# Performance work log

Hardware: AMD Instinct MI355X
Metric: run time of the kernel (lower is better)

The kernel has to match this reference:

```python
import jax, jax.numpy as jnp
import numpy as np

# Mamba2 defaults (mamba_ssm): d_state=128, d_conv=4, expand=2, headdim=64, ngroups=1
NB, D_MODEL, D_STATE, D_CONV, HEADDIM = 2, 512, 128, 4, 64
D_INNER = 2 * D_MODEL                      # expand * d_model
NHEADS = D_INNER // HEADDIM                # 16
CONV_DIM = D_INNER + 2 * D_STATE           # x, B, C go through depthwise conv
D_IN_PROJ = 2 * D_INNER + 2 * D_STATE + NHEADS  # z, xBC, dt
VOCAB, LABEL, B, L = 32000, 1000, 2, 512


def setup_inputs() -> dict:
    key = jax.random.key(0)
    ks = jax.random.split(key, 8)
    nrm = lambda k, shape, s: jax.random.normal(k, shape, dtype=jnp.float32) * s
    tokens = jax.random.randint(ks[0], (B, L), 0, VOCAB)
    embedding = nrm(ks[1], (VOCAB, D_MODEL), 0.02)
    in_proj_w = nrm(ks[2], (NB, D_IN_PROJ, D_MODEL), D_MODEL ** -0.5)
    conv_w = nrm(ks[3], (NB, CONV_DIM, D_CONV), D_CONV ** -0.5)
    conv_b = jnp.zeros((NB, CONV_DIM), jnp.float32)
    # dt_bias = inverse-softplus of dt ~ logUniform[1e-3, 0.1] (Mamba2 init)
    dt = jnp.exp(jax.random.uniform(ks[4], (NB, NHEADS), minval=float(np.log(1e-3)), maxval=float(np.log(0.1))))
    dt_bias = dt + jnp.log(-jnp.expm1(-dt))
    A_log = jnp.log(jax.random.uniform(ks[5], (NB, NHEADS), minval=1.0, maxval=16.0))
    D = jnp.ones((NB, NHEADS), jnp.float32)
    rms_w = jnp.ones((NB, D_INNER), jnp.float32)
    out_proj_w = nrm(ks[6], (NB, D_MODEL, D_INNER), D_INNER ** -0.5)
    ln_w = jnp.ones((NB, D_MODEL), jnp.float32)
    ln_b = jnp.zeros((NB, D_MODEL), jnp.float32)
    head_w = nrm(ks[7], (LABEL, D_MODEL), D_MODEL ** -0.5)
    head_b = jnp.zeros((LABEL,), jnp.float32)
    return dict(tokens=tokens, embedding=embedding, in_proj_w=in_proj_w, conv_w=conv_w,
                conv_b=conv_b, dt_bias=dt_bias, A_log=A_log, D=D, rms_w=rms_w,
                out_proj_w=out_proj_w, ln_w=ln_w, ln_b=ln_b, head_w=head_w, head_b=head_b)


def _mamba2(u, Wi, cw, cb, dtb, Alog, Dv, rw, Wo):
    b, l, _ = u.shape
    zxbcdt = u @ Wi.T                                  # (b,l,D_IN_PROJ)
    z = zxbcdt[..., :D_INNER]
    xBC = zxbcdt[..., D_INNER:D_INNER + CONV_DIM]
    dt = jax.nn.softplus(zxbcdt[..., D_INNER + CONV_DIM:] + dtb)   # (b,l,h)
    # causal depthwise conv1d, kernel size D_CONV
    xp = jnp.pad(xBC, ((0, 0), (D_CONV - 1, 0), (0, 0)))
    xBC = sum(xp[:, k:k + l, :] * cw[:, k] for k in range(D_CONV)) + cb
    xBC = jax.nn.silu(xBC)
    xh = xBC[..., :D_INNER].reshape(b, l, NHEADS, HEADDIM)
    Bm = xBC[..., D_INNER:D_INNER + D_STATE]           # (b,l,n), ngroups=1
    Cm = xBC[..., D_INNER + D_STATE:]                  # (b,l,n)
    A = -jnp.exp(Alog)                                 # (h,)
    dA = jnp.exp(dt * A)                               # (b,l,h)

    def step(h, inp):
        dA_t, dt_t, x_t, B_t, C_t = inp                # (b,h),(b,h),(b,h,p),(b,n),(b,n)
        h = h * dA_t[:, :, None, None] + (dt_t[:, :, None] * x_t)[..., None] * B_t[:, None, None, :]
        return h, jnp.einsum('bhpn,bn->bhp', h, C_t)

    h0 = jnp.zeros((b, NHEADS, HEADDIM, D_STATE), u.dtype)
    inp = (jnp.swapaxes(dA, 0, 1), jnp.swapaxes(dt, 0, 1), jnp.swapaxes(xh, 0, 1),
           jnp.swapaxes(Bm, 0, 1), jnp.swapaxes(Cm, 0, 1))
    _, ys = jax.lax.scan(step, h0, inp)
    y = jnp.swapaxes(ys, 0, 1) + Dv[:, None] * xh      # (b,l,h,p)
    # gated RMSNorm (norm_before_gate=False): normalize y*silu(z)
    y = y.reshape(b, l, D_INNER) * jax.nn.silu(z)
    y = y * jax.lax.rsqrt(jnp.mean(y * y, -1, keepdims=True) + 1e-5) * rw
    return y @ Wo.T


def _layernorm(x, w, bias):
    mu = jnp.mean(x, -1, keepdims=True)
    xc = x - mu
    var = jnp.mean(xc * xc, -1, keepdims=True)
    return xc * jax.lax.rsqrt(var + 1e-5) * w + bias


def reference(tokens, embedding, in_proj_w, conv_w, conv_b, dt_bias, A_log, D,
              rms_w, out_proj_w, ln_w, ln_b, head_w, head_b):
    x = embedding[tokens]                              # (b,l,d)
    for i in range(NB):
        y = _mamba2(x, in_proj_w[i], conv_w[i], conv_b[i], dt_bias[i],
                    A_log[i], D[i], rms_w[i], out_proj_w[i])
        x = _layernorm(y + x, ln_w[i], ln_b[i])        # residual + LN (dropout=identity)
    return x @ head_w.T + head_b                        # (b,l,label)
```

## Files before the change

kernel.cpp:

```cpp
#include <hip/hip_runtime.h>

#define L_SEQ 512
#define BATCH 2
#define NROWS (BATCH*L_SEQ)
#define DMODEL 512
#define DINNER 1024
#define DSTATE 128
#define NHEADSM 16
#define CONVD 1280
#define DINPROJ 2320
#define QCH 32
#define NCH 16
#define WI_PAD 2368
#define WH_PAD 1024

#define W_CONVW 0
#define W_CONVB 10240
#define W_DTB   12800
#define W_ALOG  12832
#define W_DD    12864
#define W_RMSW  12896
#define W_LNW   14944
#define W_LNB   15968
#define W_HEADB 16992
#define O_X     18048
#define O_ZX    (O_X  + NROWS*DMODEL)
#define O_XC    (O_ZX + NROWS*DINPROJ)
#define O_DT    (O_XC + NROWS*CONVD)
#define O_Y     (O_DT + NROWS*NHEADSM)
#define O_O     (O_Y  + NROWS*DINNER)
#define O_LA    (O_O  + NROWS*DMODEL)
#define O_S     (O_LA + 16384)
#define O_UB    (O_S  + 4194304)
#define U_WI   0
#define U_WO   2424832
#define U_WH   3473408
#define U_XBF  3997696
#define U_YBF  4521984

#define NSMALL 17992
#define NPREPW (2*WI_PAD + 2*DMODEL + WH_PAD)

typedef __attribute__((ext_vector_type(8))) short short8;
typedef __attribute__((ext_vector_type(4))) float floatx4;

__device__ __forceinline__ float b2f(unsigned short h){ return __uint_as_float(((unsigned)h)<<16); }
__device__ __forceinline__ unsigned short f2b(float x){
  unsigned u = __float_as_uint(x);
  return (unsigned short)((u + 0x7fffu + ((u>>16)&1u)) >> 16);
}
__device__ __forceinline__ float loadIn(const void* p, long i, int f){
  return f ? b2f(((const unsigned short*)p)[i]) : ((const float*)p)[i];
}

__global__ void k_detect(const unsigned* __restrict__ emb, int* __restrict__ flag){
  __shared__ int red[256];
  int t = threadIdx.x; int cnt = 0;
  for (int i = 0; i < 16; i++){
    unsigned w = emb[t*16 + i];
    unsigned e = (w >> 7) & 0xffu;
    cnt += (e >= 100 && e <= 126) ? 1 : 0;
  }
  red[t] = cnt; __syncthreads();
  if (t == 0){
    int s = 0;
    for (int i = 0; i < 256; i++) s += red[i];
    *flag = (s > 2048) ? 1 : 0;
  }
}

struct ConvArgs { const void* src[9]; int off[10]; };

__global__ void k_prep(ConvArgs a, const void* __restrict__ wi, const void* __restrict__ wo,
                       const void* __restrict__ wh, const int* __restrict__ tok,
                       const void* __restrict__ emb, const int* __restrict__ flag,
                       float* __restrict__ dstSmall,
                       unsigned short* __restrict__ WiB, unsigned short* __restrict__ WoB,
                       unsigned short* __restrict__ WhB,
                       float* __restrict__ x, unsigned short* __restrict__ xbf)
{
  int f = *flag;
  int blk = blockIdx.x;
  if (blk < 71){
    int i = blk*256 + threadIdx.x;
    if (i < a.off[9]){
      int s = 0;
      while (i >= a.off[s+1]) s++;
      dstSmall[i] = loadIn(a.src[s], i - a.off[s], f);
    }
    return;
  }
  blk -= 71;
  if (blk < NPREPW){
    int r = blk;
    const void* src = nullptr; unsigned short* dst; long sb = 0, db; int K; bool zero = false;
    if (r < 2*WI_PAD){
      int layer = r / WI_PAD, row = r % WI_PAD;
      K = DMODEL; dst = WiB; db = ((long)layer*WI_PAD + row)*DMODEL;
      if (row < DINPROJ){ src = wi; sb = ((long)layer*DINPROJ + row)*DMODEL; } else zero = true;
    } else if (r < 2*WI_PAD + 2*DMODEL){
      int rr = r - 2*WI_PAD;
      K = DINNER; dst = WoB; db = (long)rr*DINNER;
      src = wo; sb = db;
    } else {
      int row = r - 2*WI_PAD - 2*DMODEL;
      K = DMODEL; dst = WhB; db = (long)row*DMODEL;
      if (row < 1000){ src = wh; sb = db; } else zero = true;
    }
    for (int c = threadIdx.x; c < K; c += 256)
      dst[db + c] = zero ? (unsigned short)0
                         : (f ? ((const unsigned short*)src)[sb + c] : f2b(((const float*)src)[sb + c]));
    return;
  }
  int r = blk - NPREPW;
  long base = (long)tok[r] * DMODEL;
  for (int c = threadIdx.x; c < DMODEL; c += 256){
    float v = loadIn(emb, base + c, f);
    x[(long)r*DMODEL + c] = v;
    xbf[(long)r*DMODEL + c] = f ? ((const unsigned short*)emb)[base + c] : f2b(v);
  }
}

__global__ __launch_bounds__(256) void k_mfma_nt(
    const unsigned short* __restrict__ A, const unsigned short* __restrict__ B,
    void* __restrict__ C, int M, int N, int K,
    const float* __restrict__ bias, const int* __restrict__ flag, int outDual)
{
  __shared__ unsigned short As[4096];
  __shared__ unsigned short Bs[4096];
  int f = *flag;
  int t = threadIdx.x;
  int w = t >> 6, lane = t & 63;
  int quad = lane >> 4, l16 = lane & 15;
  int m0 = blockIdx.y << 6, n0 = blockIdx.x << 6;
  int wm = (w & 1) << 5, wn = (w >> 1) << 5;
  floatx4 acc[2][2];
  #pragma unroll
  for (int mi = 0; mi < 2; mi++)
    #pragma unroll
    for (int ni = 0; ni < 2; ni++) acc[mi][ni] = (floatx4){0.f,0.f,0.f,0.f};

  int idx0 = (w << 7) + lane;
  int r0s = idx0 >> 3, g0 = idx0 & 7;
  int idx1 = idx0 + 64;
  int r1s = idx1 >> 3, g1 = idx1 & 7;
  long aOff0 = (long)(m0 + r0s)*K + g0*8;
  long aOff1 = (long)(m0 + r1s)*K + g1*8;
  long bOff0 = (long)(n0 + r0s)*K + g0*8;
  long bOff1 = (long)(n0 + r1s)*K + g1*8;
  int w0 = r0s*64 + (g0 ^ (r0s & 7))*8;
  int w1 = r1s*64 + (g1 ^ (r1s & 7))*8;

  for (int k0 = 0; k0 < K; k0 += 64){
    short8 a0 = *(const short8*)&A[aOff0 + k0];
    short8 a1 = *(const short8*)&A[aOff1 + k0];
    short8 b0 = *(const short8*)&B[bOff0 + k0];
    short8 b1 = *(const short8*)&B[bOff1 + k0];
    __syncthreads();
    *(short8*)&As[w0] = a0; *(short8*)&As[w1] = a1;
    *(short8*)&Bs[w0] = b0; *(short8*)&Bs[w1] = b1;
    __syncthreads();
    #pragma unroll
    for (int ks = 0; ks < 2; ks++){
      short8 af[2], bfr[2];
      #pragma unroll
      for (int mi = 0; mi < 2; mi++){
        int r = wm + mi*16 + l16;
        int pos = ((ks << 2) + quad) ^ (r & 7);
        af[mi] = *(const short8*)&As[r*64 + pos*8];
      }
      #pragma unroll
      for (int ni = 0; ni < 2; ni++){
        int r = wn + ni*16 + l16;
        int pos = ((ks << 2) + quad) ^ (r & 7);
        bfr[ni] = *(const short8*)&Bs[r*64 + pos*8];
      }
      #pragma unroll
      for (int mi = 0; mi < 2; mi++)
        #pragma unroll
        for (int ni = 0; ni < 2; ni++)
          acc[mi][ni] = __builtin_amdgcn_mfma_f32_16x16x32_bf16(af[mi], bfr[ni], acc[mi][ni], 0, 0, 0);
    }
  }
  #pragma unroll
  for (int mi = 0; mi < 2; mi++)
    #pragma unroll
    for (int ni = 0; ni < 2; ni++){
      int col = n0 + wn + ni*16 + l16;
      if (col >= N) continue;
      float bv = bias ? bias[col] : 0.f;
      #pragma unroll
      for (int rr = 0; rr < 4; rr++){
        int row = m0 + wm + mi*16 + (quad << 2) + rr;
        float v = acc[mi][ni][rr] + bv;
        long idx = (long)row*N + col;
        if (outDual && f) ((unsigned short*)C)[idx] = f2b(v);
        else              ((float*)C)[idx] = v;
      }
    }
}

__global__ __launch_bounds__(256) void k_conv_dt(
    const float* __restrict__ zx, const float* __restrict__ cw, const float* __restrict__ cb,
    const float* __restrict__ dtb, float* __restrict__ xc, float* __restrict__ dt)
{
  int r = blockIdx.x; int b = r >> 9, l = r & 511;
  int t = threadIdx.x;
  for (int c = t; c < CONVD; c += 256){
    float s = cb[c];
    #pragma unroll
    for (int k = 0; k < 4; k++){
      int pos = l - 3 + k;
      if (pos >= 0)
        s = fmaf(zx[(long)(b*L_SEQ + pos)*DINPROJ + DINNER + c], cw[c*4 + k], s);
    }
    xc[(long)r*CONVD + c] = s / (1.f + __expf(-s));
  }
  if (t < NHEADSM){
    float v = zx[(long)r*DINPROJ + DINNER + CONVD + t] + dtb[t];
    dt[r*NHEADSM + t] = (v > 20.f) ? v : log1pf(__expf(v));
  }
}

__global__ __launch_bounds__(256) void k_chunk1(
    const float* __restrict__ xc, const float* __restrict__ dtbuf,
    const float* __restrict__ alog, const float* __restrict__ dvec,
    float* __restrict__ S, float* __restrict__ LAb, float* __restrict__ y)
{
  int c = blockIdx.x, h = blockIdx.y, b = blockIdx.z;
  int t = threadIdx.x, w = t >> 6, lane = t & 63;
  int quad = lane >> 4, l16 = lane & 15;
  int l0 = c*QCH;
  __shared__ unsigned short XT[64*40];
  __shared__ unsigned short BTc[128*40];
  __shared__ unsigned short Bb[32*136];
  __shared__ unsigned short Cb[32*136];
  __shared__ unsigned short Gb[32*40];
  __shared__ float dtl[32], lal[32], coef[32];
  float A  = -__expf(alog[h]);
  float Dv = dvec[h];

  float xv[8];
  #pragma unroll
  for (int k = 0; k < 8; k++){
    int idx = t + k*256; int j = idx >> 6, p = idx & 63;
    xv[k] = xc[(long)(b*L_SEQ + l0 + j)*CONVD + h*64 + p];
  }
  float bv[16], cv[16];
  #pragma unroll
  for (int k = 0; k < 16; k++){
    int idx = t + k*256; int j = idx >> 7, n = idx & 127;
    long rb = (long)(b*L_SEQ + l0 + j)*CONVD + DINNER;
    bv[k] = xc[rb + n];
    cv[k] = xc[rb + DSTATE + n];
  }
  if (t < 32) dtl[t] = dtbuf[(b*L_SEQ + l0 + t)*NHEADSM + h];
  __syncthreads();
  if (t == 0){ float s = 0.f; for (int i = 0; i < 32; i++){ s += dtl[i]; lal[i] = s*A; } }
  __syncthreads();
  if (t < 32){
    coef[t] = __expf(lal[31] - lal[t]) * dtl[t];
    LAb[(b*NHEADSM + h)*L_SEQ + l0 + t] = lal[t];
  }
  __syncthreads();
  #pragma unroll
  for (int k = 0; k < 8; k++){
    int idx = t + k*256; int j = idx >> 6, p = idx & 63;
    XT[p*40 + j] = f2b(xv[k]);
  }
  #pragma unroll
  for (int k = 0; k < 16; k++){
    int idx = t + k*256; int j = idx >> 7, n = idx & 127;
    Bb[j*136 + n] = f2b(bv[k]);
    Cb[j*136 + n] = f2b(cv[k]);
    BTc[n*40 + j] = f2b(bv[k] * coef[j]);
  }
  __syncthreads();

  short8 afS = *(const short8*)&XT[(w*16 + l16)*40 + quad*8];
  floatx4 accS[8];
  #pragma unroll
  for (int nb = 0; nb < 8; nb++){
    short8 bfS = *(const short8*)&BTc[(nb*16 + l16)*40 + quad*8];
    accS[nb] = __builtin_amdgcn_mfma_f32_16x16x32_bf16(afS, bfS, (floatx4){0.f,0.f,0.f,0.f}, 0, 0, 0);
  }
  int ti = w & 1, tj = w >> 1;
  floatx4 accG = (floatx4){0.f,0.f,0.f,0.f};
  #pragma unroll
  for (int ks = 0; ks < 4; ks++){
    short8 ga = *(const short8*)&Cb[(ti*16 + l16)*136 + ks*32 + quad*8];
    short8 gb = *(const short8*)&Bb[(tj*16 + l16)*136 + ks*32 + quad*8];
    accG = __builtin_amdgcn_mfma_f32_16x16x32_bf16(ga, gb, accG, 0, 0, 0);
  }
  long sb = ((long)((b*NHEADSM + h)*NCH + c))*8192;
  #pragma unroll
  for (int nb = 0; nb < 8; nb++)
    #pragma unroll
    for (int rr = 0; rr < 4; rr++)
      S[sb + (w*16 + quad*4 + rr)*128 + nb*16 + l16] = accS[nb][rr];
  #pragma unroll
  for (int rr = 0; rr < 4; rr++){
    int i = ti*16 + quad*4 + rr, j = tj*16 + l16;
    float g = (j <= i) ? __expf(lal[i] - lal[j]) * dtl[j] * accG[rr] : 0.f;
    Gb[i*40 + j] = f2b(g);
  }
  __syncthreads();
  short8 ag = *(const short8*)&Gb[(ti*16 + l16)*40 + quad*8];
  #pragma unroll
  for (int s = 0; s < 2; s++){
    int pb = (w >> 1)*2 + s;
    short8 bx = *(const short8*)&XT[(pb*16 + l16)*40 + quad*8];
    floatx4 accY = __builtin_amdgcn_mfma_f32_16x16x32_bf16(ag, bx, (floatx4){0.f,0.f,0.f,0.f}, 0, 0, 0);
    #pragma unroll
    for (int rr = 0; rr < 4; rr++){
      int i = ti*16 + quad*4 + rr, p = pb*16 + l16;
      float xval = b2f(XT[p*40 + i]);
      y[(long)(b*L_SEQ + l0 + i)*DINNER + h*64 + p] = fmaf(Dv, xval, accY[rr]);
    }
  }
}

__global__ __launch_bounds__(256) void k_chunk2(
    float* __restrict__ S, const float* __restrict__ LAb)
{
  int bh = blockIdx.x >> 5;
  int e = ((blockIdx.x & 31) << 8) + threadIdx.x;
  long base = (long)bh*NCH*8192 + e;
  int laBase = bh*L_SEQ;
  float lam[NCH];
  #pragma unroll
  for (int c = 0; c < NCH; c++) lam[c] = __expf(LAb[laBase + c*QCH + QCH - 1]);
  float hr = 0.f;
  #pragma unroll
  for (int c = 0; c < NCH; c++){
    long off = base + (long)c*8192;
    float sv = S[off];
    S[off] = hr;
    hr = fmaf(hr, lam[c], sv);
  }
}

__global__ __launch_bounds__(256) void k_chunk3(
    const float* __restrict__ xc, const float* __restrict__ H,
    const float* __restrict__ LAb, float* __restrict__ y)
{
  int c = blockIdx.x, h = blockIdx.y, b = blockIdx.z;
  int t = threadIdx.x, w = t >> 6, lane = t & 63;
  int quad = lane >> 4, l16 = lane & 15;
  int l0 = c*QCH;
  __shared__ unsigned short Cb[32*136];
  __shared__ unsigned short Hhi[64*136];
  __shared__ unsigned short Hlo[64*136];
  __shared__ float el[32];
  if (t < 32) el[t] = __expf(LAb[(b*NHEADSM + h)*L_SEQ + l0 + t]);
  #pragma unroll
  for (int k = 0; k < 16; k++){
    int idx = t + k*256; int j = idx >> 7, n = idx & 127;
    Cb[j*136 + n] = f2b(xc[(long)(b*L_SEQ + l0 + j)*CONVD + DINNER + DSTATE + n]);
  }
  long hb = ((long)((b*NHEADSM + h)*NCH + c))*8192;
  #pragma unroll
  for (int k = 0; k < 32; k++){
    int idx = t + k*256; int p = idx >> 7, n = idx & 127;
    float v = H[hb + idx];
    unsigned short hi = f2b(v);
    Hhi[p*136 + n] = hi;
    Hlo[p*136 + n] = f2b(v - b2f(hi));
  }
  __syncthreads();
  int ti = w & 1;
  #pragma unroll
  for (int s = 0; s < 2; s++){
    int pb = (w >> 1)*2 + s;
    floatx4 acc = (floatx4){0.f,0.f,0.f,0.f};
    #pragma unroll
    for (int ks = 0; ks < 4; ks++){
      short8 a  = *(const short8*)&Cb [(ti*16 + l16)*136 + ks*32 + quad*8];
      short8 bl = *(const short8*)&Hlo[(pb*16 + l16)*136 + ks*32 + quad*8];
      short8 bh = *(const short8*)&Hhi[(pb*16 + l16)*136 + ks*32 + quad*8];
      acc = __builtin_amdgcn_mfma_f32_16x16x32_bf16(a, bl, acc, 0, 0, 0);
      acc = __builtin_amdgcn_mfma_f32_16x16x32_bf16(a, bh, acc, 0, 0, 0);
    }
    #pragma unroll
    for (int rr = 0; rr < 4; rr++){
      int i = ti*16 + quad*4 + rr, p = pb*16 + l16;
      long yb = (long)(b*L_SEQ + l0 + i)*DINNER + h*64 + p;
      y[yb] = fmaf(el[i], acc[rr], y[yb]);
    }
  }
}

__global__ __launch_bounds__(256) void k_gated_rms(
    const float* __restrict__ y, const float* __restrict__ zx, const float* __restrict__ rw,
    unsigned short* __restrict__ ybf)
{
  int r = blockIdx.x, t = threadIdx.x;
  float g[4]; float ss = 0.f;
  #pragma unroll
  for (int i = 0; i < 4; i++){
    int c = t + i*256;
    float z  = zx[(long)r*DINPROJ + c];
    float yv = y[(long)r*DINNER + c];
    float gz = z / (1.f + __expf(-z));
    g[i] = yv * gz;
    ss = fmaf(g[i], g[i], ss);
  }
  #pragma unroll
  for (int o = 1; o < 64; o <<= 1) ss += __shfl_xor(ss, o);
  __shared__ float red[4];
  int w = t >> 6, lane = t & 63;
  if (lane == 0) red[w] = ss;
  __syncthreads();
  float tot = red[0] + red[1] + red[2] + red[3];
  float sc = rsqrtf(tot / (float)DINNER + 1e-5f);
  #pragma unroll
  for (int i = 0; i < 4; i++){
    int c = t + i*256;
    ybf[(long)r*DINNER + c] = f2b(g[i] * sc * rw[c]);
  }
}

__global__ __launch_bounds__(256) void k_add_ln(
    float* __restrict__ x, const float* __restrict__ o,
    const float* __restrict__ lw, const float* __restrict__ lb,
    unsigned short* __restrict__ xbf)
{
  int r = blockIdx.x, t = threadIdx.x;
  float v[2]; float sm = 0.f;
  #pragma unroll
  for (int i = 0; i < 2; i++){ int c = t + i*256; v[i] = x[(long)r*DMODEL + c] + o[(long)r*DMODEL + c]; sm += v[i]; }
  #pragma unroll
  for (int off = 1; off < 64; off <<= 1) sm += __shfl_xor(sm, off);
  __shared__ float red[4]; __shared__ float red2[4];
  int w = t >> 6, lane = t & 63;
  if (lane == 0) red[w] = sm;
  __syncthreads();
  float mu = (red[0] + red[1] + red[2] + red[3]) / (float)DMODEL;
  float var = 0.f;
  #pragma unroll
  for (int i = 0; i < 2; i++){ v[i] -= mu; var = fmaf(v[i], v[i], var); }
  #pragma unroll
  for (int off = 1; off < 64; off <<= 1) var += __shfl_xor(var, off);
  if (lane == 0) red2[w] = var;
  __syncthreads();
  float vv = (red2[0] + red2[1] + red2[2] + red2[3]) / (float)DMODEL;
  float sc = rsqrtf(vv + 1e-5f);
  #pragma unroll
  for (int i = 0; i < 2; i++){
    int c = t + i*256;
    float ov = v[i]*sc*lw[c] + lb[c];
    x[(long)r*DMODEL + c] = ov;
    xbf[(long)r*DMODEL + c] = f2b(ov);
  }
}

extern "C" void kernel_launch(void* const* d_in, const int* in_sizes, int n_in,
                              void* d_out, int out_size, void* d_ws, size_t ws_size,
                              hipStream_t stream)
{
  const int* tokens = (const int*)d_in[0];
  const void* emb = d_in[1];
  int* flag = (int*)d_ws;
  float* ws = (float*)((char*)d_ws + 256);

  k_detect<<<1, 256, 0, stream>>>((const unsigned*)emb, flag);

  ConvArgs ca;
  const int sizes[9] = {10240, 2560, 32, 32, 32, 2048, 1024, 1024, 1000};
  const int idxs[9]  = {3, 4, 5, 6, 7, 8, 10, 11, 13};
  int off = 0;
  for (int s = 0; s < 9; s++){ ca.src[s] = d_in[idxs[s]]; ca.off[s] = off; off += sizes[s]; }
  ca.off[9] = off;

  float* X  = ws + O_X;
  float* ZX = ws + O_ZX;
  float* XC = ws + O_XC;
  float* DT = ws + O_DT;
  float* Y  = ws + O_Y;
  float* Ob = ws + O_O;
  float* LA = ws + O_LA;
  float* Sb = ws + O_S;
  unsigned short* ub  = (unsigned short*)(ws + O_UB);
  unsigned short* WiB = ub + U_WI;
  unsigned short* WoB = ub + U_WO;
  unsigned short* WhB = ub + U_WH;
  unsigned short* Xbf = ub + U_XBF;
  unsigned short* Ybf = ub + U_YBF;

  k_prep<<<71 + NPREPW + NROWS, 256, 0, stream>>>(
      ca, d_in[2], d_in[9], d_in[12], tokens, emb, flag,
      ws, WiB, WoB, WhB, X, Xbf);

  for (int layer = 0; layer < 2; layer++){
    k_mfma_nt<<<dim3(WI_PAD/64, NROWS/64), 256, 0, stream>>>(
        Xbf, WiB + (long)layer*WI_PAD*DMODEL, (void*)ZX,
        NROWS, DINPROJ, DMODEL, (const float*)nullptr, flag, 0);
    k_conv_dt<<<NROWS, 256, 0, stream>>>(
        ZX, ws + W_CONVW + layer*5120, ws + W_CONVB + layer*1280, ws + W_DTB + layer*16, XC, DT);
    k_chunk1<<<dim3(NCH, NHEADSM, BATCH), 256, 0, stream>>>(
        XC, DT, ws + W_ALOG + layer*16, ws + W_DD + layer*16, Sb, LA, Y);
    k_chunk2<<<1024, 256, 0, stream>>>(Sb, LA);
    k_chunk3<<<dim3(NCH, NHEADSM, BATCH), 256, 0, stream>>>(XC, Sb, LA, Y);
    k_gated_rms<<<NROWS, 256, 0, stream>>>(Y, ZX, ws + W_RMSW + layer*1024, Ybf);
    k_mfma_nt<<<dim3(DMODEL/64, NROWS/64), 256, 0, stream>>>(
        Ybf, WoB + (long)layer*DMODEL*DINNER, (void*)Ob,
        NROWS, DMODEL, DINNER, (const float*)nullptr, flag, 0);
    k_add_ln<<<NROWS, 256, 0, stream>>>(X, Ob, ws + W_LNW + layer*512, ws + W_LNB + layer*512, Xbf);
  }

  k_mfma_nt<<<dim3(WH_PAD/64, NROWS/64), 256, 0, stream>>>(
      Xbf, WhB, d_out, NROWS, 1000, DMODEL, ws + W_HEADB, flag, 1);
}
```

Before: 255.8 us.

## Fuse conv/dt into chunk kernel and merge state pass with output correction

Folds the causal depthwise conv, SiLU and dt softplus into the first chunked-scan kernel, so the XC and DT intermediates are no longer written and reread. That kernel now also stores C in bf16 for reuse. The inter-chunk state recurrence and the state-to-output correction are merged into one kernel with one block per (batch, head) that loops sequentially over the chunks. This removes two launches and the fp32 XC round trip, but the second kernel runs only 32 blocks, which leaves most of the GPU idle and serialises the work over chunks.

New measurement: 479.9 us. 87.6% more time.

```diff
diff --git a/kernel.cpp b/kernel.cpp
--- a/kernel.cpp
+++ b/kernel.cpp
@@ -38,7 +38,6 @@
 #define U_XBF  3997696
 #define U_YBF  4521984
 
-#define NSMALL 17992
 #define NPREPW (2*WI_PAD + 2*DMODEL + WH_PAD)
 
 typedef __attribute__((ext_vector_type(8))) short short8;
@@ -52,6 +51,7 @@
 __device__ __forceinline__ float loadIn(const void* p, long i, int f){
   return f ? b2f(((const unsigned short*)p)[i]) : ((const float*)p)[i];
 }
+__device__ __forceinline__ float silu(float s){ return s / (1.f + __expf(-s)); }
 
 __global__ void k_detect(const unsigned* __restrict__ emb, int* __restrict__ flag){
   __shared__ int red[256];
@@ -200,32 +200,11 @@
     }
 }
 
-__global__ __launch_bounds__(256) void k_conv_dt(
-    const float* __restrict__ zx, const float* __restrict__ cw, const float* __restrict__ cb,
-    const float* __restrict__ dtb, float* __restrict__ xc, float* __restrict__ dt)
-{
-  int r = blockIdx.x; int b = r >> 9, l = r & 511;
-  int t = threadIdx.x;
-  for (int c = t; c < CONVD; c += 256){
-    float s = cb[c];
-    #pragma unroll
-    for (int k = 0; k < 4; k++){
-      int pos = l - 3 + k;
-      if (pos >= 0)
-        s = fmaf(zx[(long)(b*L_SEQ + pos)*DINPROJ + DINNER + c], cw[c*4 + k], s);
-    }
-    xc[(long)r*CONVD + c] = s / (1.f + __expf(-s));
-  }
-  if (t < NHEADSM){
-    float v = zx[(long)r*DINPROJ + DINNER + CONVD + t] + dtb[t];
-    dt[r*NHEADSM + t] = (v > 20.f) ? v : log1pf(__expf(v));
-  }
-}
-
-__global__ __launch_bounds__(256) void k_chunk1(
-    const float* __restrict__ xc, const float* __restrict__ dtbuf,
-    const float* __restrict__ alog, const float* __restrict__ dvec,
-    float* __restrict__ S, float* __restrict__ LAb, float* __restrict__ y)
+__global__ __launch_bounds__(256) void k_scan1(
+    const float* __restrict__ zx, const float* __restrict__ cw, const float* __restrict__ cbv,
+    const float* __restrict__ dtb, const float* __restrict__ alog, const float* __restrict__ dvec,
+    float* __restrict__ S, float* __restrict__ LAb, unsigned short* __restrict__ CbS,
+    float* __restrict__ y)
 {
   int c = blockIdx.x, h = blockIdx.y, b = blockIdx.z;
   int t = threadIdx.x, w = t >> 6, lane = t & 63;
@@ -240,21 +219,10 @@
   float A  = -__expf(alog[h]);
   float Dv = dvec[h];
 
-  float xv[8];
-  #pragma unroll
-  for (int k = 0; k < 8; k++){
-    int idx = t + k*256; int j = idx >> 6, p = idx & 63;
-    xv[k] = xc[(long)(b*L_SEQ + l0 + j)*CONVD + h*64 + p];
-  }
-  float bv[16], cv[16];
-  #pragma unroll
-  for (int k = 0; k < 16; k++){
-    int idx = t + k*256; int j = idx >> 7, n = idx & 127;
-    long rb = (long)(b*L_SEQ + l0 + j)*CONVD + DINNER;
-    bv[k] = xc[rb + n];
-    cv[k] = xc[rb + DSTATE + n];
-  }
-  if (t < 32) dtl[t] = dtbuf[(b*L_SEQ + l0 + t)*NHEADSM + h];
+  if (t < 32){
+    float v = zx[(long)(b*L_SEQ + l0 + t)*DINPROJ + 2304 + h] + dtb[h];
+    dtl[t] = (v > 20.f) ? v : log1pf(__expf(v));
+  }
   __syncthreads();
   if (t == 0){ float s = 0.f; for (int i = 0; i < 32; i++){ s += dtl[i]; lal[i] = s*A; } }
   __syncthreads();
@@ -263,17 +231,51 @@
     LAb[(b*NHEADSM + h)*L_SEQ + l0 + t] = lal[t];
   }
   __syncthreads();
-  #pragma unroll
-  for (int k = 0; k < 8; k++){
-    int idx = t + k*256; int j = idx >> 6, p = idx & 63;
-    XT[p*40 + j] = f2b(xv[k]);
-  }
-  #pragma unroll
-  for (int k = 0; k < 16; k++){
-    int idx = t + k*256; int j = idx >> 7, n = idx & 127;
-    Bb[j*136 + n] = f2b(bv[k]);
-    Cb[j*136 + n] = f2b(cv[k]);
-    BTc[n*40 + j] = f2b(bv[k] * coef[j]);
+
+  int ccA = 1024 + t;
+  float cwA0 = cw[ccA*4], cwA1 = cw[ccA*4+1], cwA2 = cw[ccA*4+2], cwA3 = cw[ccA*4+3];
+  float cbA = cbv[ccA];
+  int gcA = 2048 + t;
+  float w0A = 0.f, w1A = 0.f, w2A = 0.f;
+  int ccB = h*64 + (t & 63);
+  float cwB0 = cw[ccB*4], cwB1 = cw[ccB*4+1], cwB2 = cw[ccB*4+2], cwB3 = cw[ccB*4+3];
+  float cbB = cbv[ccB];
+  int gcB = 1024 + ccB;
+  float w0B = 0.f, w1B = 0.f, w2B = 0.f;
+  long rowBase = (long)(b*L_SEQ + l0)*DINPROJ;
+  if (c > 0){
+    w0A = zx[rowBase - 3*DINPROJ + gcA];
+    w1A = zx[rowBase - 2*DINPROJ + gcA];
+    w2A = zx[rowBase - 1*DINPROJ + gcA];
+    if (t < 64){
+      w0B = zx[rowBase - 3*DINPROJ + gcB];
+      w1B = zx[rowBase - 2*DINPROJ + gcB];
+      w2B = zx[rowBase - 1*DINPROJ + gcB];
+    }
+  }
+  long cBase = ((long)((b*NHEADSM + h)*NCH + c))*4096;
+  #pragma unroll 4
+  for (int i = 0; i < 32; i++){
+    long rb = rowBase + (long)i*DINPROJ;
+    float zA = zx[rb + gcA];
+    float sA = silu(cbA + cwA0*w0A + cwA1*w1A + cwA2*w2A + cwA3*zA);
+    w0A = w1A; w1A = w2A; w2A = zA;
+    if (t < 128){
+      unsigned short bb = f2b(sA);
+      Bb[i*136 + t] = bb;
+      BTc[t*40 + i] = f2b(sA * coef[i]);
+    } else {
+      int n = t - 128;
+      unsigned short cc = f2b(sA);
+      Cb[i*136 + n] = cc;
+      CbS[cBase + i*128 + n] = cc;
+    }
+    if (t < 64){
+      float zB = zx[rb + gcB];
+      float sB = silu(cbB + cwB0*w0B + cwB1*w1B + cwB2*w2B + cwB3*zB);
+      w0B = w1B; w1B = w2B; w2B = zB;
+      XT[t*40 + i] = f2b(sB);
+    }
   }
   __syncthreads();
 
@@ -320,73 +322,68 @@
   }
 }
 
-__global__ __launch_bounds__(256) void k_chunk2(
-    float* __restrict__ S, const float* __restrict__ LAb)
-{
-  int bh = blockIdx.x >> 5;
-  int e = ((blockIdx.x & 31) << 8) + threadIdx.x;
-  long base = (long)bh*NCH*8192 + e;
-  int laBase = bh*L_SEQ;
-  float lam[NCH];
-  #pragma unroll
-  for (int c = 0; c < NCH; c++) lam[c] = __expf(LAb[laBase + c*QCH + QCH - 1]);
-  float hr = 0.f;
-  #pragma unroll
-  for (int c = 0; c < NCH; c++){
-    long off = base + (long)c*8192;
-    float sv = S[off];
-    S[off] = hr;
-    hr = fmaf(hr, lam[c], sv);
-  }
-}
-
-__global__ __launch_bounds__(256) void k_chunk3(
-    const float* __restrict__ xc, const float* __restrict__ H,
+__global__ __launch_bounds__(256) void k_scan2(
+    const unsigned short* __restrict__ CbS, const float* __restrict__ S,
     const float* __restrict__ LAb, float* __restrict__ y)
 {
-  int c = blockIdx.x, h = blockIdx.y, b = blockIdx.z;
+  int h = blockIdx.x & 15, b = blockIdx.x >> 4;
   int t = threadIdx.x, w = t >> 6, lane = t & 63;
   int quad = lane >> 4, l16 = lane & 15;
-  int l0 = c*QCH;
+  int bh = b*NHEADSM + h;
   __shared__ unsigned short Cb[32*136];
   __shared__ unsigned short Hhi[64*136];
   __shared__ unsigned short Hlo[64*136];
   __shared__ float el[32];
-  if (t < 32) el[t] = __expf(LAb[(b*NHEADSM + h)*L_SEQ + l0 + t]);
-  #pragma unroll
-  for (int k = 0; k < 16; k++){
-    int idx = t + k*256; int j = idx >> 7, n = idx & 127;
-    Cb[j*136 + n] = f2b(xc[(long)(b*L_SEQ + l0 + j)*CONVD + DINNER + DSTATE + n]);
-  }
-  long hb = ((long)((b*NHEADSM + h)*NCH + c))*8192;
-  #pragma unroll
-  for (int k = 0; k < 32; k++){
-    int idx = t + k*256; int p = idx >> 7, n = idx & 127;
-    float v = H[hb + idx];
-    unsigned short hi = f2b(v);
-    Hhi[p*136 + n] = hi;
-    Hlo[p*136 + n] = f2b(v - b2f(hi));
-  }
-  __syncthreads();
+  float hreg[32];
+  #pragma unroll
+  for (int k = 0; k < 32; k++) hreg[k] = 0.f;
+  long sBase = (long)bh*NCH*8192;
+  long cBase = (long)bh*NCH*4096;
+  int laBase = bh*L_SEQ;
   int ti = w & 1;
-  #pragma unroll
-  for (int s = 0; s < 2; s++){
-    int pb = (w >> 1)*2 + s;
-    floatx4 acc = (floatx4){0.f,0.f,0.f,0.f};
-    #pragma unroll
-    for (int ks = 0; ks < 4; ks++){
-      short8 a  = *(const short8*)&Cb [(ti*16 + l16)*136 + ks*32 + quad*8];
-      short8 bl = *(const short8*)&Hlo[(pb*16 + l16)*136 + ks*32 + quad*8];
-      short8 bh = *(const short8*)&Hhi[(pb*16 + l16)*136 + ks*32 + quad*8];
-      acc = __builtin_amdgcn_mfma_f32_16x16x32_bf16(a, bl, acc, 0, 0, 0);
-      acc = __builtin_amdgcn_mfma_f32_16x16x32_bf16(a, bh, acc, 0, 0, 0);
-    }
-    #pragma unroll
-    for (int rr = 0; rr < 4; rr++){
-      int i = ti*16 + quad*4 + rr, p = pb*16 + l16;
-      long yb = (long)(b*L_SEQ + l0 + i)*DINNER + h*64 + p;
-      y[yb] = fmaf(el[i], acc[rr], y[yb]);
-    }
+  for (int c = 0; c < NCH; c++){
+    if (t < 32) el[t] = __expf(LAb[laBase + c*QCH + t]);
+    #pragma unroll
+    for (int k = 0; k < 16; k++){
+      int idx = t + k*256; int j = idx >> 7, n = idx & 127;
+      Cb[j*136 + n] = CbS[cBase + c*4096 + idx];
+    }
+    #pragma unroll
+    for (int k = 0; k < 32; k++){
+      int idx = t + k*256; int p = idx >> 7, n = idx & 127;
+      float v = hreg[k];
+      unsigned short hi = f2b(v);
+      Hhi[p*136 + n] = hi;
+      Hlo[p*136 + n] = f2b(v - b2f(hi));
+    }
+    __syncthreads();
+    int l0 = c*QCH;
+    #pragma unroll
+    for (int s = 0; s < 2; s++){
+      int pb = (w >> 1)*2 + s;
+      floatx4 acc = (floatx4){0.f,0.f,0.f,0.f};
+      #pragma unroll
+      for (int ks = 0; ks < 4; ks++){
+        short8 a  = *(const short8*)&Cb [(ti*16 + l16)*136 + ks*32 + quad*8];
+        short8 bl = *(const short8*)&Hlo[(pb*16 + l16)*136 + ks*32 + quad*8];
+        short8 bhv= *(const short8*)&Hhi[(pb*16 + l16)*136 + ks*32 + quad*8];
+        acc = __builtin_amdgcn_mfma_f32_16x16x32_bf16(a, bl, acc, 0, 0, 0);
+        acc = __builtin_amdgcn_mfma_f32_16x16x32_bf16(a, bhv, acc, 0, 0, 0);
+      }
+      #pragma unroll
+      for (int rr = 0; rr < 4; rr++){
+        int i = ti*16 + quad*4 + rr, p = pb*16 + l16;
+        long yb = (long)(b*L_SEQ + l0 + i)*DINNER + h*64 + p;
+        y[yb] = fmaf(el[i], acc[rr], y[yb]);
+      }
+    }
+    float lam = __expf(LAb[laBase + c*QCH + QCH - 1]);
+    #pragma unroll
+    for (int k = 0; k < 32; k++){
+      float sv = S[sBase + (long)c*8192 + t + k*256];
+      hreg[k] = fmaf(hreg[k], lam, sv);
+    }
+    __syncthreads();
   }
 }
 
@@ -401,8 +398,7 @@
     int c = t + i*256;
     float z  = zx[(long)r*DINPROJ + c];
     float yv = y[(long)r*DINNER + c];
-    float gz = z / (1.f + __expf(-z));
-    g[i] = yv * gz;
+    g[i] = yv * silu(z);
     ss = fmaf(g[i], g[i], ss);
   }
   #pragma unroll
@@ -474,12 +470,11 @@
 
   float* X  = ws + O_X;
   float* ZX = ws + O_ZX;
-  float* XC = ws + O_XC;
-  float* DT = ws + O_DT;
   float* Y  = ws + O_Y;
   float* Ob = ws + O_O;
   float* LA = ws + O_LA;
   float* Sb = ws + O_S;
+  unsigned short* CbS = (unsigned short*)(ws + O_XC);
   unsigned short* ub  = (unsigned short*)(ws + O_UB);
   unsigned short* WiB = ub + U_WI;
   unsigned short* WoB = ub + U_WO;
@@ -495,12 +490,10 @@
     k_mfma_nt<<<dim3(WI_PAD/64, NROWS/64), 256, 0, stream>>>(
         Xbf, WiB + (long)layer*WI_PAD*DMODEL, (void*)ZX,
         NROWS, DINPROJ, DMODEL, (const float*)nullptr, flag, 0);
-    k_conv_dt<<<NROWS, 256, 0, stream>>>(
-        ZX, ws + W_CONVW + layer*5120, ws + W_CONVB + layer*1280, ws + W_DTB + layer*16, XC, DT);
-    k_chunk1<<<dim3(NCH, NHEADSM, BATCH), 256, 0, stream>>>(
-        XC, DT, ws + W_ALOG + layer*16, ws + W_DD + layer*16, Sb, LA, Y);
-    k_chunk2<<<1024, 256, 0, stream>>>(Sb, LA);
-    k_chunk3<<<dim3(NCH, NHEADSM, BATCH), 256, 0, stream>>>(XC, Sb, LA, Y);
+    k_scan1<<<dim3(NCH, NHEADSM, BATCH), 256, 0, stream>>>(
+        ZX, ws + W_CONVW + layer*5120, ws + W_CONVB + layer*1280, ws + W_DTB + layer*16,
+        ws + W_ALOG + layer*16, ws + W_DD + layer*16, Sb, LA, CbS, Y);
+    k_scan2<<<BATCH*NHEADSM, 256, 0, stream>>>(CbS, Sb, LA, Y);
     k_gated_rms<<<NROWS, 256, 0, stream>>>(Y, ZX, ws + W_RMSW + layer*1024, Ybf);
     k_mfma_nt<<<dim3(DMODEL/64, NROWS/64), 256, 0, stream>>>(
         Ybf, WoB + (long)layer*DMODEL*DINNER, (void*)Ob,
```
